# Kernel tuning notes

Hardware: AMD Instinct MI355X
Metric: run time of the kernel (lower is better)

Reference implementation:

```python
import jax, jax.numpy as jnp
import numpy as np

EPS = 1e-15
BALL_EPS = 1e-5  # geoopt-style clamp away from the ball boundary


def expmap0(u):
    # Poincare ball (curvature -1): expmap0(u) = tanh(||u||) * u / ||u||
    n = jnp.linalg.norm(u, axis=-1, keepdims=True)
    n = jnp.maximum(n, EPS)
    return jnp.tanh(n) * u / n


def setup_inputs() -> dict:
    key = jax.random.key(0)
    k1, k2, k3 = jax.random.split(key, 3)
    B, H, D, L = 32768, 768, 384, 128
    cls_output = jax.random.normal(k1, (B, H), dtype=jnp.float32)
    W_proj = jax.random.normal(k2, (H, D), dtype=jnp.float32) * 0.02
    b_proj = jnp.zeros((D,), dtype=jnp.float32)
    # class prototypes: uniform(-0.1, 0.1) then expmap0, as in __init__
    tangent = jax.random.uniform(k3, (L, D), dtype=jnp.float32, minval=-0.1, maxval=0.1)
    poincare_weight = expmap0(tangent)
    return {"cls_output": cls_output, "W_proj": W_proj, "b_proj": b_proj,
            "poincare_weight": poincare_weight}


def reference(cls_output, W_proj, b_proj, poincare_weight):
    # projection (dropout is identity in eval mode)
    projected = cls_output @ W_proj + b_proj            # [B, D]
    x = expmap0(projected)                              # [B, D] points in ball
    y = poincare_weight                                 # [L, D] class reps in ball
    # Poincare distance for all (B, L) pairs, fused via dot products:
    # ||(-x) mobius+ y||^2 = ||x - y||^2 / (1 - 2<x,y> + ||x||^2 ||y||^2)
    x2 = jnp.sum(x * x, axis=-1)                        # [B]
    y2 = jnp.sum(y * y, axis=-1)                        # [L]
    xy = x @ y.T                                        # [B, L]
    sq_diff = x2[:, None] + y2[None, :] - 2.0 * xy      # ||x - y||^2
    denom = 1.0 - 2.0 * xy + x2[:, None] * y2[None, :]
    ratio = jnp.clip(sq_diff / denom, 0.0, (1.0 - BALL_EPS) ** 2)
    dist = 2.0 * jnp.arctanh(jnp.sqrt(ratio))           # [B, L]
    logits = -dist
    return logits, x
```

## Files before the change

### kernel.cpp

```cpp
#include <hip/hip_runtime.h>

typedef __attribute__((ext_vector_type(8))) short bf16x8;
typedef __attribute__((ext_vector_type(16))) float f32x16;

__device__ __forceinline__ unsigned short f2b(float f) {
  unsigned x = __builtin_bit_cast(unsigned, f);
  x += 0x7fffu + ((x >> 16) & 1u);
  return (unsigned short)(x >> 16);
}

__global__ __launch_bounds__(256) void k_prep(const float* __restrict__ W,
                                              const float* __restrict__ Y,
                                              unsigned short* __restrict__ Wt,
                                              unsigned short* __restrict__ Ybf,
                                              float* __restrict__ y2) {
  __shared__ unsigned short sT[64][72];
  int b = blockIdx.x;
  if (b < 72) {
    int bk = (b % 12) * 64, bn = (b / 12) * 64;
    int c = threadIdx.x & 63, rr = threadIdx.x >> 6;
#pragma unroll
    for (int i = 0; i < 16; i++) {
      int row = rr * 16 + i;
      sT[row][c] = f2b(W[(size_t)(bk + row) * 384 + bn + c]);
    }
    __syncthreads();
#pragma unroll
    for (int i = 0; i < 16; i++) {
      int row = rr * 16 + i;
      Wt[(size_t)(bn + row) * 768 + bk + c] = sT[c][row];
    }
  } else {
    int t = threadIdx.x;
    for (int i = t; i < 12288; i += 256) {
      float4 v = ((const float4*)Y)[i];
      ushort4 o;
      o.x = f2b(v.x); o.y = f2b(v.y); o.z = f2b(v.z); o.w = f2b(v.w);
      ((ushort4*)Ybf)[i] = o;
    }
    if (t < 128) {
      const float4* row = (const float4*)(Y + (size_t)t * 384);
      float s = 0.f;
#pragma unroll
      for (int j = 0; j < 96; j++) {
        float4 v = row[j];
        s += v.x * v.x + v.y * v.y + v.z * v.z + v.w * v.w;
      }
      y2[t] = s;
    }
  }
}

#define LDS1 72
#define LDSX 392
#define LDSY 136

__global__ __launch_bounds__(512, 2) void k_main(const float* __restrict__ cls,
                                                 const unsigned short* __restrict__ Wt,
                                                 const float* __restrict__ bias,
                                                 const unsigned short* __restrict__ Ybf,
                                                 const float* __restrict__ y2,
                                                 float* __restrict__ xout,
                                                 float* __restrict__ out) {
  __shared__ __align__(16) unsigned short sm[50176 + 17408];
  __shared__ float rs[128][4];
  __shared__ float sF[128];
  __shared__ float sQ[128];

  unsigned short* sA = sm;
  unsigned short* sW = sm + 9216;
  unsigned short* sX = sm;
  unsigned short* sY = sm + 50176;

  const int tid = threadIdx.x;
  const int bm = blockIdx.x * 128;
  const int wave = tid >> 6, lane = tid & 63;
  const int r = lane & 31, h = lane >> 5;
  const int rg = wave & 1, cg = wave >> 1;

  f32x16 acc[2][3];
#pragma unroll
  for (int i = 0; i < 2; i++)
#pragma unroll
    for (int j = 0; j < 3; j++)
#pragma unroll
      for (int e = 0; e < 16; e++) acc[i][j][e] = 0.f;

  float4 rA[2][2];
  uint4 rW[6];

#pragma unroll
  for (int it = 0; it < 2; it++) {
    int c = tid + it * 512, row = c >> 3, kc = c & 7;
    const float* src = cls + (size_t)(bm + row) * 768 + kc * 8;
    rA[it][0] = *(const float4*)(src);
    rA[it][1] = *(const float4*)(src + 4);
  }
#pragma unroll
  for (int it = 0; it < 6; it++) {
    int c = tid + it * 512, row = c >> 3, kc = c & 7;
    rW[it] = *(const uint4*)(Wt + (size_t)row * 768 + kc * 8);
  }

  for (int t = 0; t < 12; t++) {
    asm volatile("s_waitcnt lgkmcnt(0)" ::: "memory");
    __builtin_amdgcn_s_barrier();

#pragma unroll
    for (int it = 0; it < 2; it++) {
      int c = tid + it * 512, row = c >> 3, kc = c & 7;
      uint4 p;
      p.x = (unsigned)f2b(rA[it][0].x) | ((unsigned)f2b(rA[it][0].y) << 16);
      p.y = (unsigned)f2b(rA[it][0].z) | ((unsigned)f2b(rA[it][0].w) << 16);
      p.z = (unsigned)f2b(rA[it][1].x) | ((unsigned)f2b(rA[it][1].y) << 16);
      p.w = (unsigned)f2b(rA[it][1].z) | ((unsigned)f2b(rA[it][1].w) << 16);
      *(uint4*)(sA + row * LDS1 + kc * 8) = p;
    }
#pragma unroll
    for (int it = 0; it < 6; it++) {
      int c = tid + it * 512, row = c >> 3, kc = c & 7;
      *(uint4*)(sW + row * LDS1 + kc * 8) = rW[it];
    }

    if (t < 11) {
      const int k0 = (t + 1) * 64;
#pragma unroll
      for (int it = 0; it < 2; it++) {
        int c = tid + it * 512, row = c >> 3, kc = c & 7;
        const float* src = cls + (size_t)(bm + row) * 768 + k0 + kc * 8;
        rA[it][0] = *(const float4*)(src);
        rA[it][1] = *(const float4*)(src + 4);
      }
#pragma unroll
      for (int it = 0; it < 6; it++) {
        int c = tid + it * 512, row = c >> 3, kc = c & 7;
        rW[it] = *(const uint4*)(Wt + (size_t)row * 768 + k0 + kc * 8);
      }
    }

    asm volatile("s_waitcnt lgkmcnt(0)" ::: "memory");
    __builtin_amdgcn_s_barrier();

#pragma unroll
    for (int sub = 0; sub < 4; sub++) {
      const int kk = sub * 16 + h * 8;
      bf16x8 a0 = *(const bf16x8*)(sA + (rg * 64 + r) * LDS1 + kk);
      bf16x8 a1 = *(const bf16x8*)(sA + (rg * 64 + 32 + r) * LDS1 + kk);
      bf16x8 b0 = *(const bf16x8*)(sW + (cg * 96 + r) * LDS1 + kk);
      bf16x8 b1 = *(const bf16x8*)(sW + (cg * 96 + 32 + r) * LDS1 + kk);
      bf16x8 b2 = *(const bf16x8*)(sW + (cg * 96 + 64 + r) * LDS1 + kk);
      acc[0][0] = __builtin_amdgcn_mfma_f32_32x32x16_bf16(a0, b0, acc[0][0], 0, 0, 0);
      acc[0][1] = __builtin_amdgcn_mfma_f32_32x32x16_bf16(a0, b1, acc[0][1], 0, 0, 0);
      acc[0][2] = __builtin_amdgcn_mfma_f32_32x32x16_bf16(a0, b2, acc[0][2], 0, 0, 0);
      acc[1][0] = __builtin_amdgcn_mfma_f32_32x32x16_bf16(a1, b0, acc[1][0], 0, 0, 0);
      acc[1][1] = __builtin_amdgcn_mfma_f32_32x32x16_bf16(a1, b1, acc[1][1], 0, 0, 0);
      acc[1][2] = __builtin_amdgcn_mfma_f32_32x32x16_bf16(a1, b2, acc[1][2], 0, 0, 0);
    }
  }

  float bcol[3];
#pragma unroll
  for (int j = 0; j < 3; j++) bcol[j] = bias[cg * 96 + j * 32 + r];

#pragma unroll
  for (int i = 0; i < 2; i++) {
#pragma unroll
    for (int reg = 0; reg < 16; reg++) {
      float s = 0.f;
#pragma unroll
      for (int j = 0; j < 3; j++) {
        float v = acc[i][j][reg] + bcol[j];
        acc[i][j][reg] = v;
        s += v * v;
      }
      s += __shfl_xor(s, 1);
      s += __shfl_xor(s, 2);
      s += __shfl_xor(s, 4);
      s += __shfl_xor(s, 8);
      s += __shfl_xor(s, 16);
      if (r == 0) {
        int rowl = rg * 64 + i * 32 + (reg & 3) + 8 * (reg >> 2) + 4 * h;
        rs[rowl][cg] = s;
      }
    }
  }
  __syncthreads();
  if (tid < 128) {
    float n2 = rs[tid][0] + rs[tid][1] + rs[tid][2] + rs[tid][3];
    float n = fmaxf(sqrtf(n2), 1e-15f);
    float f = tanhf(n) / n;
    sF[tid] = f;
    sQ[tid] = n2 * f * f;
  }
  __syncthreads();

#pragma unroll
  for (int i = 0; i < 2; i++) {
#pragma unroll
    for (int reg = 0; reg < 16; reg++) {
      int rowl = rg * 64 + i * 32 + (reg & 3) + 8 * (reg >> 2) + 4 * h;
      float f = sF[rowl];
#pragma unroll
      for (int j = 0; j < 3; j++) {
        float v = acc[i][j][reg] * f;
        xout[(size_t)(bm + rowl) * 384 + cg * 96 + j * 32 + r] = v;
        sX[rowl * LDSX + cg * 96 + j * 32 + r] = f2b(v);
      }
    }
  }

  const int rt = 32 * (wave & 3), ct = 64 * (wave >> 2);
  f32x16 acc2[2];
#pragma unroll
  for (int j = 0; j < 2; j++)
#pragma unroll
    for (int e = 0; e < 16; e++) acc2[j][e] = 0.f;

  for (int k0 = 0; k0 < 384; k0 += 128) {
    asm volatile("s_waitcnt lgkmcnt(0)" ::: "memory");
    __builtin_amdgcn_s_barrier();
#pragma unroll
    for (int c = tid; c < 2048; c += 512) {
      int row = c >> 4, kc = c & 15;
      *(uint4*)(sY + row * LDSY + kc * 8) =
          *(const uint4*)(Ybf + (size_t)row * 384 + k0 + kc * 8);
    }
    asm volatile("s_waitcnt lgkmcnt(0)" ::: "memory");
    __builtin_amdgcn_s_barrier();
#pragma unroll
    for (int sub = 0; sub < 8; sub++) {
      const int kk = sub * 16 + h * 8;
      bf16x8 a = *(const bf16x8*)(sX + (rt + r) * LDSX + k0 + kk);
      bf16x8 b0 = *(const bf16x8*)(sY + (ct + r) * LDSY + kk);
      bf16x8 b1 = *(const bf16x8*)(sY + (ct + 32 + r) * LDSY + kk);
      acc2[0] = __builtin_amdgcn_mfma_f32_32x32x16_bf16(a, b0, acc2[0], 0, 0, 0);
      acc2[1] = __builtin_amdgcn_mfma_f32_32x32x16_bf16(a, b1, acc2[1], 0, 0, 0);
    }
  }

  const float CLIP = 0.9999800001f;
  float yc[2] = {y2[ct + r], y2[ct + 32 + r]};
#pragma unroll
  for (int reg = 0; reg < 16; reg++) {
    int rowl = rt + (reg & 3) + 8 * (reg >> 2) + 4 * h;
    float xr = sQ[rowl];
#pragma unroll
    for (int j = 0; j < 2; j++) {
      float xy = acc2[j][reg];
      float sq = xr + yc[j] - 2.f * xy;
      float den = 1.f - 2.f * xy + xr * yc[j];
      float ratio = fminf(fmaxf(sq / den, 0.f), CLIP);
      float s = sqrtf(ratio);
      float dist = logf((1.f + s) / (1.f - s));
      out[(size_t)(bm + rowl) * 128 + ct + j * 32 + r] = -dist;
    }
  }
}

extern "C" void kernel_launch(void* const* d_in, const int* in_sizes, int n_in,
                              void* d_out, int out_size, void* d_ws, size_t ws_size,
                              hipStream_t stream) {
  const float* cls  = (const float*)d_in[0];
  const float* W    = (const float*)d_in[1];
  const float* bias = (const float*)d_in[2];
  const float* Y    = (const float*)d_in[3];

  float* out_logits = (float*)d_out;
  float* out_x = out_logits + (size_t)32768 * 128;

  float* x2 = (float*)d_ws;
  float* y2 = x2 + 32768;
  unsigned short* Wt = (unsigned short*)(y2 + 128);
  unsigned short* Ybf = Wt + (size_t)384 * 768;

  k_prep<<<73, 256, 0, stream>>>(W, Y, Wt, Ybf, y2);
  k_main<<<256, 512, 0, stream>>>(cls, Wt, bias, Ybf, y2, out_x, out_logits);
}
```

Measured before the change: 240.1 us.

## Halve row tile, swizzle LDS layout, raise occupancy, prefetch Y tiles

The row tile per block drops from 128 to 64, giving 512 blocks, and launch bounds rise to 4 blocks per CU. The smaller shared-memory footprint is what lets more blocks fit on each CU. Padded LDS rows are replaced with an XOR swizzle to avoid bank conflicts, and the second GEMM now register-prefetches the Y tiles in 64-wide chunks. The aim is better latency hiding and more parallelism across 256 CUs. The cost is that each Wt tile gets reused across only half as many rows, which doubles weight traffic per output row.

```diff
diff --git a/kernel.cpp b/kernel.cpp
--- a/kernel.cpp
+++ b/kernel.cpp
@@ -51,50 +51,45 @@
   }
 }
 
-#define LDS1 72
-#define LDSX 392
-#define LDSY 136
-
-__global__ __launch_bounds__(512, 2) void k_main(const float* __restrict__ cls,
+#define SWZ(row, slot) ((((row) << 3) + ((slot) ^ ((row) & 7))) << 3)
+
+__global__ __launch_bounds__(512, 4) void k_main(const float* __restrict__ cls,
                                                  const unsigned short* __restrict__ Wt,
                                                  const float* __restrict__ bias,
                                                  const unsigned short* __restrict__ Ybf,
                                                  const float* __restrict__ y2,
                                                  float* __restrict__ xout,
                                                  float* __restrict__ out) {
-  __shared__ __align__(16) unsigned short sm[50176 + 17408];
-  __shared__ float rs[128][4];
-  __shared__ float sF[128];
-  __shared__ float sQ[128];
+  __shared__ __align__(16) unsigned short sm[36864];
+  __shared__ float rs[64][4];
+  __shared__ float sF[64];
+  __shared__ float sQ[64];
 
   unsigned short* sA = sm;
-  unsigned short* sW = sm + 9216;
+  unsigned short* sW = sm + 4096;
   unsigned short* sX = sm;
-  unsigned short* sY = sm + 50176;
+  unsigned short* sY = sm + 28672;
 
   const int tid = threadIdx.x;
-  const int bm = blockIdx.x * 128;
+  const int bm = blockIdx.x * 64;
   const int wave = tid >> 6, lane = tid & 63;
   const int r = lane & 31, h = lane >> 5;
   const int rg = wave & 1, cg = wave >> 1;
 
-  f32x16 acc[2][3];
-#pragma unroll
-  for (int i = 0; i < 2; i++)
-#pragma unroll
-    for (int j = 0; j < 3; j++)
-#pragma unroll
-      for (int e = 0; e < 16; e++) acc[i][j][e] = 0.f;
-
-  float4 rA[2][2];
+  f32x16 acc[3];
+#pragma unroll
+  for (int j = 0; j < 3; j++)
+#pragma unroll
+    for (int e = 0; e < 16; e++) acc[j][e] = 0.f;
+
+  const int arow = tid >> 3, akc = tid & 7;
+
+  float4 rA0, rA1;
   uint4 rW[6];
-
-#pragma unroll
-  for (int it = 0; it < 2; it++) {
-    int c = tid + it * 512, row = c >> 3, kc = c & 7;
-    const float* src = cls + (size_t)(bm + row) * 768 + kc * 8;
-    rA[it][0] = *(const float4*)(src);
-    rA[it][1] = *(const float4*)(src + 4);
+  {
+    const float* src = cls + (size_t)(bm + arow) * 768 + akc * 8;
+    rA0 = *(const float4*)(src);
+    rA1 = *(const float4*)(src + 4);
   }
 #pragma unroll
   for (int it = 0; it < 6; it++) {
@@ -106,31 +101,25 @@
     asm volatile("s_waitcnt lgkmcnt(0)" ::: "memory");
     __builtin_amdgcn_s_barrier();
 
-#pragma unroll
-    for (int it = 0; it < 2; it++) {
-      int c = tid + it * 512, row = c >> 3, kc = c & 7;
+    {
       uint4 p;
-      p.x = (unsigned)f2b(rA[it][0].x) | ((unsigned)f2b(rA[it][0].y) << 16);
-      p.y = (unsigned)f2b(rA[it][0].z) | ((unsigned)f2b(rA[it][0].w) << 16);
-      p.z = (unsigned)f2b(rA[it][1].x) | ((unsigned)f2b(rA[it][1].y) << 16);
-      p.w = (unsigned)f2b(rA[it][1].z) | ((unsigned)f2b(rA[it][1].w) << 16);
-      *(uint4*)(sA + row * LDS1 + kc * 8) = p;
+      p.x = (unsigned)f2b(rA0.x) | ((unsigned)f2b(rA0.y) << 16);
+      p.y = (unsigned)f2b(rA0.z) | ((unsigned)f2b(rA0.w) << 16);
+      p.z = (unsigned)f2b(rA1.x) | ((unsigned)f2b(rA1.y) << 16);
+      p.w = (unsigned)f2b(rA1.z) | ((unsigned)f2b(rA1.w) << 16);
+      *(uint4*)(sA + SWZ(arow, akc)) = p;
     }
 #pragma unroll
     for (int it = 0; it < 6; it++) {
       int c = tid + it * 512, row = c >> 3, kc = c & 7;
-      *(uint4*)(sW + row * LDS1 + kc * 8) = rW[it];
+      *(uint4*)(sW + SWZ(row, kc)) = rW[it];
     }
 
     if (t < 11) {
       const int k0 = (t + 1) * 64;
-#pragma unroll
-      for (int it = 0; it < 2; it++) {
-        int c = tid + it * 512, row = c >> 3, kc = c & 7;
-        const float* src = cls + (size_t)(bm + row) * 768 + k0 + kc * 8;
-        rA[it][0] = *(const float4*)(src);
-        rA[it][1] = *(const float4*)(src + 4);
-      }
+      const float* src = cls + (size_t)(bm + arow) * 768 + k0 + akc * 8;
+      rA0 = *(const float4*)(src);
+      rA1 = *(const float4*)(src + 4);
 #pragma unroll
       for (int it = 0; it < 6; it++) {
         int c = tid + it * 512, row = c >> 3, kc = c & 7;
@@ -143,19 +132,22 @@
 
 #pragma unroll
     for (int sub = 0; sub < 4; sub++) {
-      const int kk = sub * 16 + h * 8;
-      bf16x8 a0 = *(const bf16x8*)(sA + (rg * 64 + r) * LDS1 + kk);
-      bf16x8 a1 = *(const bf16x8*)(sA + (rg * 64 + 32 + r) * LDS1 + kk);
-      bf16x8 b0 = *(const bf16x8*)(sW + (cg * 96 + r) * LDS1 + kk);
-      bf16x8 b1 = *(const bf16x8*)(sW + (cg * 96 + 32 + r) * LDS1 + kk);
-      bf16x8 b2 = *(const bf16x8*)(sW + (cg * 96 + 64 + r) * LDS1 + kk);
-      acc[0][0] = __builtin_amdgcn_mfma_f32_32x32x16_bf16(a0, b0, acc[0][0], 0, 0, 0);
-      acc[0][1] = __builtin_amdgcn_mfma_f32_32x32x16_bf16(a0, b1, acc[0][1], 0, 0, 0);
-      acc[0][2] = __builtin_amdgcn_mfma_f32_32x32x16_bf16(a0, b2, acc[0][2], 0, 0, 0);
-      acc[1][0] = __builtin_amdgcn_mfma_f32_32x32x16_bf16(a1, b0, acc[1][0], 0, 0, 0);
-      acc[1][1] = __builtin_amdgcn_mfma_f32_32x32x16_bf16(a1, b1, acc[1][1], 0, 0, 0);
-      acc[1][2] = __builtin_amdgcn_mfma_f32_32x32x16_bf16(a1, b2, acc[1][2], 0, 0, 0);
-    }
+      const int slot = sub * 2 + h;
+      bf16x8 a  = *(const bf16x8*)(sA + SWZ(rg * 32 + r, slot));
+      bf16x8 b0 = *(const bf16x8*)(sW + SWZ(cg * 96 + r, slot));
+      bf16x8 b1 = *(const bf16x8*)(sW + SWZ(cg * 96 + 32 + r, slot));
+      bf16x8 b2 = *(const bf16x8*)(sW + SWZ(cg * 96 + 64 + r, slot));
+      acc[0] = __builtin_amdgcn_mfma_f32_32x32x16_bf16(a, b0, acc[0], 0, 0, 0);
+      acc[1] = __builtin_amdgcn_mfma_f32_32x32x16_bf16(a, b1, acc[1], 0, 0, 0);
+      acc[2] = __builtin_amdgcn_mfma_f32_32x32x16_bf16(a, b2, acc[2], 0, 0, 0);
+    }
+  }
+
+  uint4 rY[2];
+#pragma unroll
+  for (int it = 0; it < 2; it++) {
+    int idx = tid + it * 512, row = idx >> 3, kc = idx & 7;
+    rY[it] = *(const uint4*)(Ybf + (size_t)row * 384 + kc * 8);
   }
 
   float bcol[3];
@@ -163,29 +155,26 @@
   for (int j = 0; j < 3; j++) bcol[j] = bias[cg * 96 + j * 32 + r];
 
 #pragma unroll
-  for (int i = 0; i < 2; i++) {
-#pragma unroll
-    for (int reg = 0; reg < 16; reg++) {
-      float s = 0.f;
-#pragma unroll
-      for (int j = 0; j < 3; j++) {
-        float v = acc[i][j][reg] + bcol[j];
-        acc[i][j][reg] = v;
-        s += v * v;
-      }
-      s += __shfl_xor(s, 1);
-      s += __shfl_xor(s, 2);
-      s += __shfl_xor(s, 4);
-      s += __shfl_xor(s, 8);
-      s += __shfl_xor(s, 16);
-      if (r == 0) {
-        int rowl = rg * 64 + i * 32 + (reg & 3) + 8 * (reg >> 2) + 4 * h;
-        rs[rowl][cg] = s;
-      }
+  for (int reg = 0; reg < 16; reg++) {
+    float s = 0.f;
+#pragma unroll
+    for (int j = 0; j < 3; j++) {
+      float v = acc[j][reg] + bcol[j];
+      acc[j][reg] = v;
+      s += v * v;
+    }
+    s += __shfl_xor(s, 1);
+    s += __shfl_xor(s, 2);
+    s += __shfl_xor(s, 4);
+    s += __shfl_xor(s, 8);
+    s += __shfl_xor(s, 16);
+    if (r == 0) {
+      int rowl = rg * 32 + (reg & 3) + 8 * (reg >> 2) + 4 * h;
+      rs[rowl][cg] = s;
     }
   }
   __syncthreads();
-  if (tid < 128) {
+  if (tid < 64) {
     float n2 = rs[tid][0] + rs[tid][1] + rs[tid][2] + rs[tid][3];
     float n = fmaxf(sqrtf(n2), 1e-15f);
     float f = tanhf(n) / n;
@@ -195,65 +184,65 @@
   __syncthreads();
 
 #pragma unroll
-  for (int i = 0; i < 2; i++) {
-#pragma unroll
-    for (int reg = 0; reg < 16; reg++) {
-      int rowl = rg * 64 + i * 32 + (reg & 3) + 8 * (reg >> 2) + 4 * h;
-      float f = sF[rowl];
-#pragma unroll
-      for (int j = 0; j < 3; j++) {
-        float v = acc[i][j][reg] * f;
-        xout[(size_t)(bm + rowl) * 384 + cg * 96 + j * 32 + r] = v;
-        sX[rowl * LDSX + cg * 96 + j * 32 + r] = f2b(v);
+  for (int reg = 0; reg < 16; reg++) {
+    int rowl = rg * 32 + (reg & 3) + 8 * (reg >> 2) + 4 * h;
+    float f = sF[rowl];
+#pragma unroll
+    for (int j = 0; j < 3; j++) {
+      float v = acc[j][reg] * f;
+      int col = cg * 96 + j * 32 + r;
+      xout[(size_t)(bm + rowl) * 384 + col] = v;
+      int slot = col >> 3, off = col & 7;
+      sX[rowl * 384 + ((slot ^ (rowl & 7)) << 3) + off] = f2b(v);
+    }
+  }
+
+  const int rt = (wave & 1) * 32, ct = (wave >> 1) * 32;
+  f32x16 acc2;
+#pragma unroll
+  for (int e = 0; e < 16; e++) acc2[e] = 0.f;
+
+  for (int c = 0; c < 6; c++) {
+    asm volatile("s_waitcnt lgkmcnt(0)" ::: "memory");
+    __builtin_amdgcn_s_barrier();
+#pragma unroll
+    for (int it = 0; it < 2; it++) {
+      int idx = tid + it * 512, row = idx >> 3, kc = idx & 7;
+      *(uint4*)(sY + SWZ(row, kc)) = rY[it];
+    }
+    if (c < 5) {
+      const int k0 = (c + 1) * 64;
+#pragma unroll
+      for (int it = 0; it < 2; it++) {
+        int idx = tid + it * 512, row = idx >> 3, kc = idx & 7;
+        rY[it] = *(const uint4*)(Ybf + (size_t)row * 384 + k0 + kc * 8);
       }
     }
-  }
-
-  const int rt = 32 * (wave & 3), ct = 64 * (wave >> 2);
-  f32x16 acc2[2];
-#pragma unroll
-  for (int j = 0; j < 2; j++)
-#pragma unroll
-    for (int e = 0; e < 16; e++) acc2[j][e] = 0.f;
-
-  for (int k0 = 0; k0 < 384; k0 += 128) {
-    asm volatile("s_waitcnt lgkmcnt(0)" ::: "memory");
-    __builtin_amdgcn_s_barrier();
-#pragma unroll
-    for (int c = tid; c < 2048; c += 512) {
-      int row = c >> 4, kc = c & 15;
-      *(uint4*)(sY + row * LDSY + kc * 8) =
-          *(const uint4*)(Ybf + (size_t)row * 384 + k0 + kc * 8);
-    }
-    asm volatile("s_waitcnt lgkmcnt(0)" ::: "memory");
-    __builtin_amdgcn_s_barrier();
-#pragma unroll
-    for (int sub = 0; sub < 8; sub++) {
-      const int kk = sub * 16 + h * 8;
-      bf16x8 a = *(const bf16x8*)(sX + (rt + r) * LDSX + k0 + kk);
-      bf16x8 b0 = *(const bf16x8*)(sY + (ct + r) * LDSY + kk);
-      bf16x8 b1 = *(const bf16x8*)(sY + (ct + 32 + r) * LDSY + kk);
-      acc2[0] = __builtin_amdgcn_mfma_f32_32x32x16_bf16(a, b0, acc2[0], 0, 0, 0);
-      acc2[1] = __builtin_amdgcn_mfma_f32_32x32x16_bf16(a, b1, acc2[1], 0, 0, 0);
+    asm volatile("s_waitcnt lgkmcnt(0)" ::: "memory");
+    __builtin_amdgcn_s_barrier();
+#pragma unroll
+    for (int sub = 0; sub < 4; sub++) {
+      const int slot = sub * 2 + h;
+      const int xs = c * 8 + slot;
+      bf16x8 a = *(const bf16x8*)(sX + (rt + r) * 384 + ((xs ^ ((rt + r) & 7)) << 3));
+      bf16x8 b = *(const bf16x8*)(sY + SWZ(ct + r, slot));
+      acc2 = __builtin_amdgcn_mfma_f32_32x32x16_bf16(a, b, acc2, 0, 0, 0);
     }
   }
 
   const float CLIP = 0.9999800001f;
-  float yc[2] = {y2[ct + r], y2[ct + 32 + r]};
+  float yc = y2[ct + r];
 #pragma unroll
   for (int reg = 0; reg < 16; reg++) {
     int rowl = rt + (reg & 3) + 8 * (reg >> 2) + 4 * h;
     float xr = sQ[rowl];
-#pragma unroll
-    for (int j = 0; j < 2; j++) {
-      float xy = acc2[j][reg];
-      float sq = xr + yc[j] - 2.f * xy;
-      float den = 1.f - 2.f * xy + xr * yc[j];
-      float ratio = fminf(fmaxf(sq / den, 0.f), CLIP);
-      float s = sqrtf(ratio);
-      float dist = logf((1.f + s) / (1.f - s));
-      out[(size_t)(bm + rowl) * 128 + ct + j * 32 + r] = -dist;
-    }
+    float xy = acc2[reg];
+    float sq = xr + yc - 2.f * xy;
+    float den = 1.f - 2.f * xy + xr * yc;
+    float ratio = fminf(fmaxf(sq / den, 0.f), CLIP);
+    float s = sqrtf(ratio);
+    float dist = logf((1.f + s) / (1.f - s));
+    out[(size_t)(bm + rowl) * 128 + ct + r] = -dist;
   }
 }
 
@@ -274,5 +263,5 @@
   unsigned short* Ybf = Wt + (size_t)384 * 768;
 
   k_prep<<<73, 256, 0, stream>>>(W, Y, Wt, Ybf, y2);
-  k_main<<<256, 512, 0, stream>>>(cls, Wt, bias, Ybf, y2, out_x, out_logits);
-}
+  k_main<<<512, 512, 0, stream>>>(cls, Wt, bias, Ybf, y2, out_x, out_logits);
+}
```

Result: slower. 298.9 us (+24.5%).
